# Kernel tuning notes

Measured on AMD Instinct MI355X. Metric: run time of the kernel, lower is better.

Reference implementation:

```python
import jax, jax.numpy as jnp
import numpy as np

B = 262144
MA = [128, 128]
MB = [128, 128]


def krone_linear(x_a, x_b, wa, wb, ba, bb):
    # slice inputs to each branch's in_features (torch slices the wider branch)
    ia, ib = wa.shape[1], wb.shape[1]
    x_a = x_a[:, :ia]
    x_b = x_b[:, :ib]
    h_a = x_a @ wa.T + ba
    h_b = x_b @ wb.T + bb
    # zero-pad the narrower output so both branches share a width (static shapes)
    oa, ob = wa.shape[0], wb.shape[0]
    if oa > ob:
        h_b = jnp.pad(h_b, ((0, 0), (0, oa - ob)))
    elif ob > oa:
        h_a = jnp.pad(h_a, ((0, 0), (0, ob - oa)))
    return h_a, h_b


def krone_softmax(x_a, x_b, fa, fb):
    x_a = x_a[:, :fa]
    x_b = x_b[:, :fb]
    # vectorized per-row Kronecker product: kron(a, b)[i*fb + j] = a[i]*b[j]
    y = (x_a[:, :, None] * x_b[:, None, :]).reshape(x_a.shape[0], fa * fb)
    return jax.nn.softmax(y, axis=1)


def setup_inputs() -> dict:
    key = jax.random.key(0)
    ks = jax.random.split(key, 13)
    s = 0.1
    inp = {
        "x": jax.random.normal(ks[0], (2, B, 2), dtype=jnp.float32),
        "w1a": jax.random.normal(ks[1], (MA[0], 2), dtype=jnp.float32) * s,
        "w1b": jax.random.normal(ks[2], (MB[0], 2), dtype=jnp.float32) * s,
        "b1a": jax.random.normal(ks[3], (MA[0],), dtype=jnp.float32) * s,
        "b1b": jax.random.normal(ks[4], (MB[0],), dtype=jnp.float32) * s,
        "w2a": jax.random.normal(ks[5], (MA[1], MA[0]), dtype=jnp.float32) * s,
        "w2b": jax.random.normal(ks[6], (MB[1], MB[0]), dtype=jnp.float32) * s,
        "b2a": jax.random.normal(ks[7], (MA[1],), dtype=jnp.float32) * s,
        "b2b": jax.random.normal(ks[8], (MB[1],), dtype=jnp.float32) * s,
        "w3a": jax.random.normal(ks[9], (1, MA[1]), dtype=jnp.float32) * s,
        "w3b": jax.random.normal(ks[10], (3, MB[1]), dtype=jnp.float32) * s,
        "b3a": jax.random.normal(ks[11], (1,), dtype=jnp.float32) * s,
        "b3b": jax.random.normal(ks[12], (3,), dtype=jnp.float32) * s,
    }
    return inp


def reference(x, w1a, w1b, b1a, b1b, w2a, w2b, b2a, b2b, w3a, w3b, b3a, b3b):
    x_a, x_b = x[0], x[1]
    h_a, h_b = krone_linear(x_a, x_b, w1a, w1b, b1a, b1b)
    h_a, h_b = jax.nn.relu(h_a), jax.nn.relu(h_b)
    h_a, h_b = krone_linear(h_a, h_b, w2a, w2b, b2a, b2b)
    h_a, h_b = jax.nn.relu(h_a), jax.nn.relu(h_b)
    h_a, h_b = krone_linear(h_a, h_b, w3a, w3b, b3a, b3b)
    return krone_softmax(h_a, h_b, 1, 3)
```

## Files before the change

### kernel.cpp

```cpp
#include <hip/hip_runtime.h>
#include <hip/hip_bf16.h>


#define BTOT 262144
#define NBLK (BTOT / 512)

typedef __attribute__((ext_vector_type(4))) float floatx4;
typedef __attribute__((ext_vector_type(8))) short bf16x8;
typedef __attribute__((ext_vector_type(4))) int  intx4;

#define OFF_W2    0
#define OFF_W1FA  32768
#define OFF_W1FB  40960
#define OFF_B2A   49152
#define OFF_B2B   49664
#define OFF_W3A   50176
#define OFF_W3T   50688
#define OFF_SA    52736
#define LDS_TOTAL 54784

static __device__ __forceinline__ int pack2bf(float lo, float hi) {
    int r;
    asm("v_cvt_pk_bf16_f32 %0, %1, %2" : "=v"(r) : "v"(lo), "v"(hi));
    return r;
}

template <int CTRL>
static __device__ __forceinline__ float dppadd(float v) {
    int t = __builtin_amdgcn_update_dpp(0, __builtin_bit_cast(int, v),
                                        CTRL, 0xF, 0xF, true);
    return v + __builtin_bit_cast(float, t);
}

static __device__ __forceinline__ float red4(float a0, float a1, float a2,
                                             float a3, int col) {
    float s0 = dppadd<0xB1>(a0), s1 = dppadd<0xB1>(a1);
    float s2 = dppadd<0xB1>(a2), s3 = dppadd<0xB1>(a3);
    float u0 = (col & 1) ? s1 : s0;
    float u1 = (col & 1) ? s3 : s2;
    float v0 = dppadd<0x4E>(u0), v1 = dppadd<0x4E>(u1);
    float w  = (col & 2) ? v1 : v0;
    w = dppadd<0x124>(w);
    w = dppadd<0x128>(w);
    return w;
}

static __device__ __forceinline__ void pack_w2(
        unsigned char* dst, int tid, const float* __restrict__ w2) {
    const float4* w2p = (const float4*)w2;
    #pragma unroll
    for (int i = 0; i < 8; ++i) {
        int n  = (tid & 15) | (i << 4);
        int k4 = tid >> 4;
        float4 f = w2p[n * 32 + k4];
        int k = k4 * 4;
        int s = k >> 5;
        int j0 = k & 7;
        int l = ((k & 31) >> 3) * 16 + (n & 15);
        int2 pkd;
        pkd.x = pack2bf(f.x, f.y);
        pkd.y = pack2bf(f.z, f.w);
        *(int2*)(dst + (s * 8 + (n >> 4)) * 1024 + l * 16 + j0 * 2) = pkd;
    }
}

static __device__ __forceinline__ void stage_w1f(
        unsigned char* smem, int off, int tid,
        const float* __restrict__ w1, const float* __restrict__ b1) {
    int tp = tid >> 6, l = tid & 63;
    intx4 e = (intx4){0, 0, 0, 0};
    if (l < 16) {
        int n1 = (tp >> 1) * 32 + (l >> 2) * 8 + (tp & 1) * 4 + (l & 3);
        float w0 = w1[2 * n1], w1v = w1[2 * n1 + 1], bb = b1[n1];
        int dhi = pack2bf(w0, w1v);
        float w0r = __builtin_bit_cast(float, dhi << 16);
        float w1r = __builtin_bit_cast(float, dhi & 0xffff0000);
        int dlo = pack2bf(w0 - w0r, w1v - w1r);
        int bh  = pack2bf(bb, 0.f);
        float bbr = __builtin_bit_cast(float, bh << 16);
        int dbias = pack2bf(bb, bb - bbr);
        e = (intx4){dhi, dlo, dhi, dbias};
    }
    ((intx4*)(smem + off))[tid] = e;
}

#define GEMM_CHUNK(acc, XF, W1Fp, W2p, B2p)                                    \
    {                                                                          \
        _Pragma("unroll")                                                      \
        for (int t = 0; t < 8; ++t) {                                          \
            float b2n = (B2p)[t * 16 + col];                                   \
            floatx4 bi = (floatx4){b2n, b2n, b2n, b2n};                        \
            _Pragma("unroll")                                                  \
            for (int mt = 0; mt < 2; ++mt) acc[t][mt] = bi;                    \
        }                                                                      \
        const floatx4 zf = (floatx4){0.f, 0.f, 0.f, 0.f};                      \
        _Pragma("unroll")                                                      \
        for (int s = 0; s < 4; ++s) {                                          \
            bf16x8 a0 = (W1Fp)[(2 * s) * 64 + lane];                           \
            bf16x8 a1 = (W1Fp)[(2 * s + 1) * 64 + lane];                       \
            intx4 af[2];                                                       \
            _Pragma("unroll")                                                  \
            for (int mt = 0; mt < 2; ++mt) {                                   \
                floatx4 td0 = __builtin_amdgcn_mfma_f32_16x16x32_bf16(         \
                    a0, __builtin_bit_cast(bf16x8, (XF)[mt]), zf, 0, 0, 0);    \
                floatx4 td1 = __builtin_amdgcn_mfma_f32_16x16x32_bf16(         \
                    a1, __builtin_bit_cast(bf16x8, (XF)[mt]), zf, 0, 0, 0);    \
                af[mt][0] = pack2bf(fmaxf(td0[0], 0.f), fmaxf(td0[1], 0.f));   \
                af[mt][1] = pack2bf(fmaxf(td0[2], 0.f), fmaxf(td0[3], 0.f));   \
                af[mt][2] = pack2bf(fmaxf(td1[0], 0.f), fmaxf(td1[1], 0.f));   \
                af[mt][3] = pack2bf(fmaxf(td1[2], 0.f), fmaxf(td1[3], 0.f));   \
            }                                                                  \
            _Pragma("unroll")                                                  \
            for (int t = 0; t < 8; ++t) {                                      \
                bf16x8 bfr = (W2p)[(s * 8 + t) * 64 + lane];                   \
                _Pragma("unroll")                                              \
                for (int mt = 0; mt < 2; ++mt)                                 \
                    acc[t][mt] = __builtin_amdgcn_mfma_f32_16x16x32_bf16(      \
                        __builtin_bit_cast(bf16x8, af[mt]), bfr,               \
                        acc[t][mt], 0, 0, 0);                                  \
            }                                                                  \
        }                                                                      \
    }

static __device__ __forceinline__ intx4 make_xfrag(float2 xx) {
    int d0 = pack2bf(xx.x, xx.y);
    float r0 = __builtin_bit_cast(float, d0 << 16);
    float r1 = __builtin_bit_cast(float, d0 & 0xffff0000);
    int d2 = pack2bf(xx.x - r0, xx.y - r1);
    return (intx4){d0, d0, d2, 0x3f803f80};
}

__global__ __launch_bounds__(512, 4)
void krone_fused(const float* __restrict__ x,
                 const float* __restrict__ w1a, const float* __restrict__ w1b,
                 const float* __restrict__ b1a, const float* __restrict__ b1b,
                 const float* __restrict__ w2a, const float* __restrict__ w2b,
                 const float* __restrict__ b2a, const float* __restrict__ b2b,
                 const float* __restrict__ w3a, const float* __restrict__ w3b,
                 const float* __restrict__ b3a, const float* __restrict__ b3b,
                 float* __restrict__ out) {
    __shared__ __align__(16) unsigned char smem[LDS_TOTAL];

    const int tid  = threadIdx.x;
    const int lane = tid & 63;
    const int wave = tid >> 6;
    const int quad = lane >> 4;
    const int col  = lane & 15;
    const int wbase = blockIdx.x * 512 + wave * 64;

    const bf16x8* W2   = (const bf16x8*)(smem + OFF_W2);
    const bf16x8* W1FA = (const bf16x8*)(smem + OFF_W1FA);
    const bf16x8* W1FB = (const bf16x8*)(smem + OFF_W1FB);
    const float*  B2A  = (const float*)(smem + OFF_B2A);
    const float*  B2B  = (const float*)(smem + OFF_B2B);
    const float*  W3A  = (const float*)(smem + OFF_W3A);
    const floatx4* W3T = (const floatx4*)(smem + OFF_W3T);
    float*        SA   = (float*)(smem + OFF_SA);
    const float2* xA = (const float2*)x;
    const float2* xB = xA + BTOT;

    const float b3a_ = b3a[0];
    const float b30 = b3b[0], b31 = b3b[1], b32 = b3b[2];

    float2 xv[4];
    #pragma unroll
    for (int c = 0; c < 2; ++c)
        #pragma unroll
        for (int mt = 0; mt < 2; ++mt)
            xv[c * 2 + mt] = xA[wbase + c * 32 + mt * 16 + col];

    pack_w2(smem + OFF_W2, tid, w2a);
    stage_w1f(smem, OFF_W1FA, tid, w1a, b1a);
    stage_w1f(smem, OFF_W1FB, tid, w1b, b1b);
    if (tid < 128) {
        ((float*)(smem + OFF_B2A))[tid] = b2a[tid];
        ((float*)(smem + OFF_B2B))[tid] = b2b[tid];
        ((float*)(smem + OFF_W3A))[tid] = w3a[tid];
    }
    if (tid < 384) {
        int j = tid >> 7, n = tid & 127;
        ((float*)(smem + OFF_W3T))[n * 4 + j] = w3b[tid];
    }
    __syncthreads();

    #pragma unroll
    for (int c = 0; c < 2; ++c) {
        intx4 xf[2];
        #pragma unroll
        for (int mt = 0; mt < 2; ++mt) xf[mt] = make_xfrag(xv[c * 2 + mt]);
        floatx4 acc[8][2];
        GEMM_CHUNK(acc, xf, W1FA, W2, B2A);

        float pa[2][4] = {};
        #pragma unroll
        for (int t = 0; t < 8; ++t) {
            float w3n = W3A[t * 16 + col];
            #pragma unroll
            for (int mt = 0; mt < 2; ++mt)
                #pragma unroll
                for (int r = 0; r < 4; ++r)
                    pa[mt][r] = fmaf(w3n, fmaxf(acc[t][mt][r], 0.f), pa[mt][r]);
        }
        #pragma unroll
        for (int mt = 0; mt < 2; ++mt) {
            float w = red4(pa[mt][0], pa[mt][1], pa[mt][2], pa[mt][3], col);
            if (col < 4) {
                int sl = mt * 16 + quad * 4 + col;
                SA[wave * 64 + c * 32 + sl] = (w + b3a_) * 1.44269504089f;
            }
        }
    }

    #pragma unroll
    for (int c = 0; c < 2; ++c)
        #pragma unroll
        for (int mt = 0; mt < 2; ++mt)
            xv[c * 2 + mt] = xB[wbase + c * 32 + mt * 16 + col];

    __syncthreads();
    pack_w2(smem + OFF_W2, tid, w2b);
    __syncthreads();

    #pragma unroll
    for (int c = 0; c < 2; ++c) {
        intx4 xf[2];
        #pragma unroll
        for (int mt = 0; mt < 2; ++mt) xf[mt] = make_xfrag(xv[c * 2 + mt]);
        floatx4 acc[8][2];
        GEMM_CHUNK(acc, xf, W1FB, W2, B2B);

        #pragma unroll
        for (int mt = 0; mt < 2; ++mt) {
            float p0[4] = {}, p1[4] = {}, p2[4] = {};
            #pragma unroll
            for (int t = 0; t < 8; ++t) {
                floatx4 w3v = W3T[t * 16 + col];
                #pragma unroll
                for (int r = 0; r < 4; ++r) {
                    float h = fmaxf(acc[t][mt][r], 0.f);
                    p0[r] = fmaf(w3v.x, h, p0[r]);
                    p1[r] = fmaf(w3v.y, h, p1[r]);
                    p2[r] = fmaf(w3v.z, h, p2[r]);
                }
            }
            float t0 = red4(p0[0], p0[1], p0[2], p0[3], col) + b30;
            float t1 = red4(p1[0], p1[1], p1[2], p1[3], col) + b31;
            float t2 = red4(p2[0], p2[1], p2[2], p2[3], col) + b32;
            if (col < 4) {
                int sl = mt * 16 + quad * 4 + col;
                float sa = SA[wave * 64 + c * 32 + sl];
                float y0 = sa * t0, y1 = sa * t1, y2 = sa * t2;
                float m = fmaxf(y0, fmaxf(y1, y2));
                float e0 = exp2f(y0 - m), e1 = exp2f(y1 - m), e2 = exp2f(y2 - m);
                float rs = __builtin_amdgcn_rcpf(e0 + e1 + e2);
                long o = (long)(wbase + c * 32 + sl) * 3;
                out[o]     = e0 * rs;
                out[o + 1] = e1 * rs;
                out[o + 2] = e2 * rs;
            }
        }
    }
}

extern "C" void kernel_launch(void* const* d_in, const int* in_sizes, int n_in,
                              void* d_out, int out_size, void* d_ws, size_t ws_size,
                              hipStream_t stream) {
    const float* x   = (const float*)d_in[0];
    const float* w1a = (const float*)d_in[1];
    const float* w1b = (const float*)d_in[2];
    const float* b1a = (const float*)d_in[3];
    const float* b1b = (const float*)d_in[4];
    const float* w2a = (const float*)d_in[5];
    const float* w2b = (const float*)d_in[6];
    const float* b2a = (const float*)d_in[7];
    const float* b2b = (const float*)d_in[8];
    const float* w3a = (const float*)d_in[9];
    const float* w3b = (const float*)d_in[10];
    const float* b3a = (const float*)d_in[11];
    const float* b3b = (const float*)d_in[12];
    float* out = (float*)d_out;

    krone_fused<<<NBLK, 512, 0, stream>>>(x, w1a, w1b, b1a, b1b, w2a, w2b,
                                          b2a, b2b, w3a, w3b, b3a, b3b, out);
}
```

Baseline: 106.2 us.

## Restructure layer-2 GEMM loop to compute per-output-tile and fuse layer-3 epilogue

The loop nest is reordered. Layer-1 activations for all four K-slices are computed first and held as packed bf16 fragments. Layer 2 then runs one 16-column output tile at a time, and each tile's result is folded straight into the layer-3 dot products. This replaces the 8x2 floatx4 accumulator array (64 VGPRs) with two live accumulators, which lowers register pressure for the 512x4 launch bounds. The cost is a serial MFMA dependency chain per tile and more interleaving between MFMA and VALU work.

```diff
diff --git a/kernel.cpp b/kernel.cpp
--- a/kernel.cpp
+++ b/kernel.cpp
@@ -84,51 +84,50 @@
     ((intx4*)(smem + off))[tid] = e;
 }
 
-#define GEMM_CHUNK(acc, XF, W1Fp, W2p, B2p)                                    \
+static __device__ __forceinline__ intx4 make_xfrag(float2 xx) {
+    int d0 = pack2bf(xx.x, xx.y);
+    float r0 = __builtin_bit_cast(float, d0 << 16);
+    float r1 = __builtin_bit_cast(float, d0 & 0xffff0000);
+    int d2 = pack2bf(xx.x - r0, xx.y - r1);
+    return (intx4){d0, d0, d2, 0x3f803f80};
+}
+
+#define LAYER1_ALL(af, XF, W1Fp)                                               \
     {                                                                          \
-        _Pragma("unroll")                                                      \
-        for (int t = 0; t < 8; ++t) {                                          \
-            float b2n = (B2p)[t * 16 + col];                                   \
-            floatx4 bi = (floatx4){b2n, b2n, b2n, b2n};                        \
-            _Pragma("unroll")                                                  \
-            for (int mt = 0; mt < 2; ++mt) acc[t][mt] = bi;                    \
-        }                                                                      \
         const floatx4 zf = (floatx4){0.f, 0.f, 0.f, 0.f};                      \
         _Pragma("unroll")                                                      \
         for (int s = 0; s < 4; ++s) {                                          \
             bf16x8 a0 = (W1Fp)[(2 * s) * 64 + lane];                           \
             bf16x8 a1 = (W1Fp)[(2 * s + 1) * 64 + lane];                       \
-            intx4 af[2];                                                       \
             _Pragma("unroll")                                                  \
             for (int mt = 0; mt < 2; ++mt) {                                   \
                 floatx4 td0 = __builtin_amdgcn_mfma_f32_16x16x32_bf16(         \
                     a0, __builtin_bit_cast(bf16x8, (XF)[mt]), zf, 0, 0, 0);    \
                 floatx4 td1 = __builtin_amdgcn_mfma_f32_16x16x32_bf16(         \
                     a1, __builtin_bit_cast(bf16x8, (XF)[mt]), zf, 0, 0, 0);    \
-                af[mt][0] = pack2bf(fmaxf(td0[0], 0.f), fmaxf(td0[1], 0.f));   \
-                af[mt][1] = pack2bf(fmaxf(td0[2], 0.f), fmaxf(td0[3], 0.f));   \
-                af[mt][2] = pack2bf(fmaxf(td1[0], 0.f), fmaxf(td1[1], 0.f));   \
-                af[mt][3] = pack2bf(fmaxf(td1[2], 0.f), fmaxf(td1[3], 0.f));   \
-            }                                                                  \
-            _Pragma("unroll")                                                  \
-            for (int t = 0; t < 8; ++t) {                                      \
-                bf16x8 bfr = (W2p)[(s * 8 + t) * 64 + lane];                   \
-                _Pragma("unroll")                                              \
-                for (int mt = 0; mt < 2; ++mt)                                 \
-                    acc[t][mt] = __builtin_amdgcn_mfma_f32_16x16x32_bf16(      \
-                        __builtin_bit_cast(bf16x8, af[mt]), bfr,               \
-                        acc[t][mt], 0, 0, 0);                                  \
+                af[s][mt][0] = pack2bf(fmaxf(td0[0], 0.f), fmaxf(td0[1], 0.f));\
+                af[s][mt][1] = pack2bf(fmaxf(td0[2], 0.f), fmaxf(td0[3], 0.f));\
+                af[s][mt][2] = pack2bf(fmaxf(td1[0], 0.f), fmaxf(td1[1], 0.f));\
+                af[s][mt][3] = pack2bf(fmaxf(td1[2], 0.f), fmaxf(td1[3], 0.f));\
             }                                                                  \
         }                                                                      \
     }
 
-static __device__ __forceinline__ intx4 make_xfrag(float2 xx) {
-    int d0 = pack2bf(xx.x, xx.y);
-    float r0 = __builtin_bit_cast(float, d0 << 16);
-    float r1 = __builtin_bit_cast(float, d0 & 0xffff0000);
-    int d2 = pack2bf(xx.x - r0, xx.y - r1);
-    return (intx4){d0, d0, d2, 0x3f803f80};
-}
+#define TTILE(acc0, acc1, af, W2p, B2p, t)                                     \
+    floatx4 acc0, acc1;                                                        \
+    {                                                                          \
+        float b2n = (B2p)[(t) * 16 + col];                                     \
+        acc0 = (floatx4){b2n, b2n, b2n, b2n};                                  \
+        acc1 = acc0;                                                           \
+        _Pragma("unroll")                                                      \
+        for (int s = 0; s < 4; ++s) {                                          \
+            bf16x8 bfr = (W2p)[(s * 8 + (t)) * 64 + lane];                     \
+            acc0 = __builtin_amdgcn_mfma_f32_16x16x32_bf16(                    \
+                __builtin_bit_cast(bf16x8, af[s][0]), bfr, acc0, 0, 0, 0);     \
+            acc1 = __builtin_amdgcn_mfma_f32_16x16x32_bf16(                    \
+                __builtin_bit_cast(bf16x8, af[s][1]), bfr, acc1, 0, 0, 0);     \
+        }                                                                      \
+    }
 
 __global__ __launch_bounds__(512, 4)
 void krone_fused(const float* __restrict__ x,
@@ -188,18 +187,19 @@
         intx4 xf[2];
         #pragma unroll
         for (int mt = 0; mt < 2; ++mt) xf[mt] = make_xfrag(xv[c * 2 + mt]);
-        floatx4 acc[8][2];
-        GEMM_CHUNK(acc, xf, W1FA, W2, B2A);
+        intx4 af[4][2];
+        LAYER1_ALL(af, xf, W1FA);
 
         float pa[2][4] = {};
         #pragma unroll
         for (int t = 0; t < 8; ++t) {
             float w3n = W3A[t * 16 + col];
+            TTILE(acc0, acc1, af, W2, B2A, t);
             #pragma unroll
-            for (int mt = 0; mt < 2; ++mt)
-                #pragma unroll
-                for (int r = 0; r < 4; ++r)
-                    pa[mt][r] = fmaf(w3n, fmaxf(acc[t][mt][r], 0.f), pa[mt][r]);
+            for (int r = 0; r < 4; ++r) {
+                pa[0][r] = fmaf(w3n, fmaxf(acc0[r], 0.f), pa[0][r]);
+                pa[1][r] = fmaf(w3n, fmaxf(acc1[r], 0.f), pa[1][r]);
+            }
         }
         #pragma unroll
         for (int mt = 0; mt < 2; ++mt) {
@@ -226,26 +226,31 @@
         intx4 xf[2];
         #pragma unroll
         for (int mt = 0; mt < 2; ++mt) xf[mt] = make_xfrag(xv[c * 2 + mt]);
-        floatx4 acc[8][2];
-        GEMM_CHUNK(acc, xf, W1FB, W2, B2B);
-
+        intx4 af[4][2];
+        LAYER1_ALL(af, xf, W1FB);
+
+        float p0[2][4] = {}, p1[2][4] = {}, p2[2][4] = {};
+        #pragma unroll
+        for (int t = 0; t < 8; ++t) {
+            floatx4 w3v = W3T[t * 16 + col];
+            TTILE(acc0, acc1, af, W2, B2B, t);
+            #pragma unroll
+            for (int r = 0; r < 4; ++r) {
+                float h0 = fmaxf(acc0[r], 0.f);
+                float h1 = fmaxf(acc1[r], 0.f);
+                p0[0][r] = fmaf(w3v.x, h0, p0[0][r]);
+                p1[0][r] = fmaf(w3v.y, h0, p1[0][r]);
+                p2[0][r] = fmaf(w3v.z, h0, p2[0][r]);
+                p0[1][r] = fmaf(w3v.x, h1, p0[1][r]);
+                p1[1][r] = fmaf(w3v.y, h1, p1[1][r]);
+                p2[1][r] = fmaf(w3v.z, h1, p2[1][r]);
+            }
+        }
         #pragma unroll
         for (int mt = 0; mt < 2; ++mt) {
-            float p0[4] = {}, p1[4] = {}, p2[4] = {};
-            #pragma unroll
-            for (int t = 0; t < 8; ++t) {
-                floatx4 w3v = W3T[t * 16 + col];
-                #pragma unroll
-                for (int r = 0; r < 4; ++r) {
-                    float h = fmaxf(acc[t][mt][r], 0.f);
-                    p0[r] = fmaf(w3v.x, h, p0[r]);
-                    p1[r] = fmaf(w3v.y, h, p1[r]);
-                    p2[r] = fmaf(w3v.z, h, p2[r]);
-                }
-            }
-            float t0 = red4(p0[0], p0[1], p0[2], p0[3], col) + b30;
-            float t1 = red4(p1[0], p1[1], p1[2], p1[3], col) + b31;
-            float t2 = red4(p2[0], p2[1], p2[2], p2[3], col) + b32;
+            float t0 = red4(p0[mt][0], p0[mt][1], p0[mt][2], p0[mt][3], col) + b30;
+            float t1 = red4(p1[mt][0], p1[mt][1], p1[mt][2], p1[mt][3], col) + b31;
+            float t2 = red4(p2[mt][0], p2[mt][1], p2[mt][2], p2[mt][3], col) + b32;
             if (col < 4) {
                 int sl = mt * 16 + quad * 4 + col;
                 float sa = SA[wave * 64 + c * 32 + sl];
```

After: 107.4 us. No clear change (+1.2%).
